# Kernel optimization log

Hardware: AMD Instinct MI355X
Metric: run time of the kernel (lower is better)

Reference implementation:

```python
import jax, jax.numpy as jnp
import numpy as np

# Module config (matches init_kwargs)
IC, OC = 8, 16
KH, KW = 3, 3
H, W = 32, 32
PAD, STRIDE = 1, 1
PH, PW = H + 2 * PAD, W + 2 * PAD          # padded input dims: 34x34
OH = (PH - KH) // STRIDE + 1                # 32
OW = (PW - KW) // STRIDE + 1                # 32
B = 64                                       # batch of flattened ciphertext images


def _build_toeplitz(kernel: np.ndarray) -> np.ndarray:
    """approximate_toeplitz_multiple_channels: dense [OC*OH*OW, IC*PH*PW] matrix
    such that T @ vec(padded_x) == vec(conv2d(x, kernel))."""
    T = np.zeros((OC * OH * OW, IC * PH * PW), dtype=np.float32)
    oh, ow = np.meshgrid(np.arange(OH), np.arange(OW), indexing="ij")
    oh, ow = oh.ravel(), ow.ravel()
    for oc in range(OC):
        rows = (oc * OH + oh) * OW + ow
        for ic in range(IC):
            for kh in range(KH):
                for kw in range(KW):
                    cols = (ic * PH + oh * STRIDE + kh) * PW + (ow * STRIDE + kw)
                    T[rows, cols] = kernel[oc, ic, kh, kw]
    return T


def _build_pad_mat() -> np.ndarray:
    """create_padding_transformation_matrix: [IC*PH*PW, IC*H*W] 0/1 matrix that
    zero-pads the flattened image (homomorphic padding as a matmul)."""
    P = np.zeros((IC * PH * PW, IC * H * W), dtype=np.float32)
    ic, h, w = np.meshgrid(np.arange(IC), np.arange(H), np.arange(W), indexing="ij")
    rows = (ic * PH + h + PAD) * PW + (w + PAD)
    cols = (ic * H + h) * W + w
    P[rows.ravel(), cols.ravel()] = 1.0
    return P


def setup_inputs() -> dict:
    rng = np.random.default_rng(0)
    kernel = rng.standard_normal((OC, IC, KH, KW)).astype(np.float32)
    weight = jnp.asarray(_build_toeplitz(kernel))                 # [OC*OH*OW, IC*PH*PW]
    bias = jnp.asarray(
        np.repeat(rng.standard_normal(OC).astype(np.float32), OH * OW)
    )                                                             # [OC*OH*OW]
    pad_mat = jnp.asarray(_build_pad_mat())                       # [IC*PH*PW, IC*H*W]
    key = jax.random.key(0)
    enc_x = jax.random.normal(key, (B, IC * H * W), dtype=jnp.float32)
    return {"enc_x": enc_x, "weight": weight, "bias": bias, "pad_mat": pad_mat}


def reference(enc_x, weight, bias, pad_mat):
    # Homomorphic conv as plaintext-equivalent math:
    # 1) pad via transformation matrix, 2) Toeplitz matmul, 3) add repeated bias.
    x_padded = enc_x @ pad_mat.T            # [B, IC*PH*PW]
    return x_padded @ weight.T + bias       # [B, OC*OH*OW]
```

## Files before the change

kernel.cpp:

```cpp
#include <hip/hip_runtime.h>

#define IC    8
#define OC    16
#define H     32
#define W     32
#define PH    34
#define PW    34
#define OH    32
#define OW    32
#define BATCH 64
#define WCOLS (IC * PH * PW)
#define XSTR  35
#define PLANE (PH * XSTR)

__global__ __launch_bounds__(256) void conv_toeplitz_kernel(
    const float* __restrict__ x,
    const float* __restrict__ weight,
    const float* __restrict__ bias,
    float* __restrict__ out)
{
    __shared__ float wk[IC * 9];
    __shared__ float xs[IC * PLANE];

    const int tid = threadIdx.x;
    const int blk = blockIdx.x;
    const int b   = blk >> 4;
    const int oc  = blk & 15;

    if (tid < IC * 9) {
        const int ic = tid / 9;
        const int k  = tid - ic * 9;
        const int kh = k / 3;
        const int kw = k - kh * 3;
        wk[tid] = weight[(size_t)(oc * OH * OW) * WCOLS + (ic * PH + kh) * PW + kw];
    }

    for (int i = tid; i < IC * PLANE; i += 256) xs[i] = 0.0f;
    __syncthreads();

    const float4* xg = (const float4*)(x + (size_t)b * (IC * H * W));
    #pragma unroll
    for (int i = 0; i < 8; ++i) {
        const int k   = tid + i * 256;
        const float4 v = xg[k];
        const int ic  = k >> 8;
        const int rem = k & 255;
        const int h   = rem >> 3;
        const int w4  = (rem & 7) << 2;
        float* dst = &xs[ic * PLANE + (h + 1) * XSTR + (w4 + 1)];
        dst[0] = v.x; dst[1] = v.y; dst[2] = v.z; dst[3] = v.w;
    }
    __syncthreads();

    float wreg[IC][3][3];
    #pragma unroll
    for (int ic = 0; ic < IC; ++ic)
        #pragma unroll
        for (int kh = 0; kh < 3; ++kh)
            #pragma unroll
            for (int kw = 0; kw < 3; ++kw)
                wreg[ic][kh][kw] = wk[ic * 9 + kh * 3 + kw];

    const int oh   = tid >> 3;
    const int ow0  = (tid & 7) << 2;
    const int oidx = oh * OW + ow0;

    const float4 bv = *(const float4*)(bias + oc * OH * OW + oidx);
    float acc0 = bv.x, acc1 = bv.y, acc2 = bv.z, acc3 = bv.w;

    #pragma unroll
    for (int ic = 0; ic < IC; ++ic) {
        #pragma unroll
        for (int kh = 0; kh < 3; ++kh) {
            const float* row = &xs[ic * PLANE + (oh + kh) * XSTR + ow0];
            const float v0 = row[0], v1 = row[1], v2 = row[2];
            const float v3 = row[3], v4 = row[4], v5 = row[5];
            const float w0 = wreg[ic][kh][0];
            const float w1 = wreg[ic][kh][1];
            const float w2 = wreg[ic][kh][2];
            acc0 += v0 * w0 + v1 * w1 + v2 * w2;
            acc1 += v1 * w0 + v2 * w1 + v3 * w2;
            acc2 += v2 * w0 + v3 * w1 + v4 * w2;
            acc3 += v3 * w0 + v4 * w1 + v5 * w2;
        }
    }

    float* op = out + (size_t)(b * OC + oc) * (OH * OW) + oidx;
    *(float4*)op = make_float4(acc0, acc1, acc2, acc3);
}

extern "C" void kernel_launch(void* const* d_in, const int* in_sizes, int n_in,
                              void* d_out, int out_size, void* d_ws, size_t ws_size,
                              hipStream_t stream) {
    const float* x      = (const float*)d_in[0];
    const float* weight = (const float*)d_in[1];
    const float* bias   = (const float*)d_in[2];
    float* out = (float*)d_out;

    conv_toeplitz_kernel<<<dim3(BATCH * OC), dim3(256), 0, stream>>>(x, weight, bias, out);
}
```

Baseline: 12.78 us.

## Compute two output channels per block and zero only the halo

Each block now computes two output channels for one image, so the staged input plane in shared memory is loaded once and reused for both, and the grid shrinks from 1024 to 512 blocks. Only the padding border is zeroed instead of the whole shared buffer, which also removes one barrier. Launch bounds now request two blocks per CU. The trade-off is more registers per thread (two weight sets and twice the accumulators) and fewer blocks to spread across the CUs.

```diff
diff --git a/kernel.cpp b/kernel.cpp
--- a/kernel.cpp
+++ b/kernel.cpp
@@ -12,31 +12,43 @@
 #define WCOLS (IC * PH * PW)
 #define XSTR  35
 #define PLANE (PH * XSTR)
+#define HALO  134
 
-__global__ __launch_bounds__(256) void conv_toeplitz_kernel(
+__global__ __launch_bounds__(256, 2) void conv_toeplitz_kernel(
     const float* __restrict__ x,
     const float* __restrict__ weight,
     const float* __restrict__ bias,
     float* __restrict__ out)
 {
-    __shared__ float wk[IC * 9];
+    __shared__ float wk[2][IC * 9];
     __shared__ float xs[IC * PLANE];
 
     const int tid = threadIdx.x;
     const int blk = blockIdx.x;
-    const int b   = blk >> 4;
-    const int oc  = blk & 15;
+    const int b   = blk >> 3;
+    const int oc0 = (blk & 7) << 1;
 
-    if (tid < IC * 9) {
-        const int ic = tid / 9;
-        const int k  = tid - ic * 9;
-        const int kh = k / 3;
-        const int kw = k - kh * 3;
-        wk[tid] = weight[(size_t)(oc * OH * OW) * WCOLS + (ic * PH + kh) * PW + kw];
+    if (tid < 144) {
+        const int os = tid / 72;
+        const int k  = tid - os * 72;
+        const int ic = k / 9;
+        const int r  = k - ic * 9;
+        const int kh = r / 3;
+        const int kw = r - kh * 3;
+        wk[os][k] = weight[(size_t)((oc0 + os) * OH * OW) * WCOLS
+                           + (ic * PH + kh) * PW + kw];
     }
 
-    for (int i = tid; i < IC * PLANE; i += 256) xs[i] = 0.0f;
-    __syncthreads();
+    for (int i = tid; i < IC * HALO; i += 256) {
+        const int plane = i / HALO;
+        const int r     = i - plane * HALO;
+        int row, col;
+        if (r < 35)       { row = 0;          col = r;        }
+        else if (r < 70)  { row = 33;         col = r - 35;   }
+        else if (r < 102) { row = r - 70 + 1; col = 0;        }
+        else              { row = r - 102 + 1; col = 33;      }
+        xs[plane * PLANE + row * XSTR + col] = 0.0f;
+    }
 
     const float4* xg = (const float4*)(x + (size_t)b * (IC * H * W));
     #pragma unroll
@@ -52,21 +64,21 @@
     }
     __syncthreads();
 
-    float wreg[IC][3][3];
+    float wreg[2][IC * 9];
     #pragma unroll
-    for (int ic = 0; ic < IC; ++ic)
+    for (int o = 0; o < 2; ++o)
         #pragma unroll
-        for (int kh = 0; kh < 3; ++kh)
-            #pragma unroll
-            for (int kw = 0; kw < 3; ++kw)
-                wreg[ic][kh][kw] = wk[ic * 9 + kh * 3 + kw];
+        for (int k = 0; k < IC * 9; ++k)
+            wreg[o][k] = wk[o][k];
 
     const int oh   = tid >> 3;
     const int ow0  = (tid & 7) << 2;
     const int oidx = oh * OW + ow0;
 
-    const float4 bv = *(const float4*)(bias + oc * OH * OW + oidx);
-    float acc0 = bv.x, acc1 = bv.y, acc2 = bv.z, acc3 = bv.w;
+    const float4 b0 = *(const float4*)(bias + oc0 * OH * OW + oidx);
+    const float4 b1 = *(const float4*)(bias + (oc0 + 1) * OH * OW + oidx);
+    float a00 = b0.x, a01 = b0.y, a02 = b0.z, a03 = b0.w;
+    float a10 = b1.x, a11 = b1.y, a12 = b1.z, a13 = b1.w;
 
     #pragma unroll
     for (int ic = 0; ic < IC; ++ic) {
@@ -75,18 +87,27 @@
             const float* row = &xs[ic * PLANE + (oh + kh) * XSTR + ow0];
             const float v0 = row[0], v1 = row[1], v2 = row[2];
             const float v3 = row[3], v4 = row[4], v5 = row[5];
-            const float w0 = wreg[ic][kh][0];
-            const float w1 = wreg[ic][kh][1];
-            const float w2 = wreg[ic][kh][2];
-            acc0 += v0 * w0 + v1 * w1 + v2 * w2;
-            acc1 += v1 * w0 + v2 * w1 + v3 * w2;
-            acc2 += v2 * w0 + v3 * w1 + v4 * w2;
-            acc3 += v3 * w0 + v4 * w1 + v5 * w2;
+            const float w00 = wreg[0][ic * 9 + kh * 3];
+            const float w01 = wreg[0][ic * 9 + kh * 3 + 1];
+            const float w02 = wreg[0][ic * 9 + kh * 3 + 2];
+            const float w10 = wreg[1][ic * 9 + kh * 3];
+            const float w11 = wreg[1][ic * 9 + kh * 3 + 1];
+            const float w12 = wreg[1][ic * 9 + kh * 3 + 2];
+            a00 += v0 * w00 + v1 * w01 + v2 * w02;
+            a01 += v1 * w00 + v2 * w01 + v3 * w02;
+            a02 += v2 * w00 + v3 * w01 + v4 * w02;
+            a03 += v3 * w00 + v4 * w01 + v5 * w02;
+            a10 += v0 * w10 + v1 * w11 + v2 * w12;
+            a11 += v1 * w10 + v2 * w11 + v3 * w12;
+            a12 += v2 * w10 + v3 * w11 + v4 * w12;
+            a13 += v3 * w10 + v4 * w11 + v5 * w12;
         }
     }
 
-    float* op = out + (size_t)(b * OC + oc) * (OH * OW) + oidx;
-    *(float4*)op = make_float4(acc0, acc1, acc2, acc3);
+    float* o0 = out + (size_t)(b * OC + oc0) * (OH * OW) + oidx;
+    *(float4*)o0 = make_float4(a00, a01, a02, a03);
+    float* o1 = o0 + OH * OW;
+    *(float4*)o1 = make_float4(a10, a11, a12, a13);
 }
 
 extern "C" void kernel_launch(void* const* d_in, const int* in_sizes, int n_in,
@@ -97,5 +118,5 @@
     const float* bias   = (const float*)d_in[2];
     float* out = (float*)d_out;
 
-    conv_toeplitz_kernel<<<dim3(BATCH * OC), dim3(256), 0, stream>>>(x, weight, bias, out);
+    conv_toeplitz_kernel<<<dim3(BATCH * (OC / 2)), dim3(256), 0, stream>>>(x, weight, bias, out);
 }
```

Result: faster. 10.94 us (-14.4%).

## Compute four output channels per block over half-image row tiles

Applied to the files above, without the earlier changes.

Each block now covers four output channels and half of the output rows (18 padded input rows), with 128 threads each producing a 4x4 register tile. Every input value loaded into shared memory is reused across four output channels, which cuts redundant input loads and shared-memory staging by roughly a factor of four. Only the halo borders are zeroed instead of the whole tile. The grid shrinks from 1024 to 512 blocks and each thread holds more accumulator and weight registers, which may reduce occupancy and latency hiding.

```diff
diff --git a/kernel.cpp b/kernel.cpp
--- a/kernel.cpp
+++ b/kernel.cpp
@@ -6,87 +6,107 @@
 #define W     32
 #define PH    34
 #define PW    34
-#define OH    32
-#define OW    32
 #define BATCH 64
 #define WCOLS (IC * PH * PW)
 #define XSTR  35
-#define PLANE (PH * XSTR)
+#define TROWS 18
+#define PLANE (TROWS * XSTR)
 
-__global__ __launch_bounds__(256) void conv_toeplitz_kernel(
+__global__ __launch_bounds__(128, 2) void conv_quad_kernel(
     const float* __restrict__ x,
     const float* __restrict__ weight,
     const float* __restrict__ bias,
     float* __restrict__ out)
 {
-    __shared__ float wk[IC * 9];
     __shared__ float xs[IC * PLANE];
+    __shared__ float wk[IC * 36];
 
-    const int tid = threadIdx.x;
+    const int t   = threadIdx.x;
     const int blk = blockIdx.x;
-    const int b   = blk >> 4;
-    const int oc  = blk & 15;
+    const int b   = blk >> 3;
+    const int q   = (blk >> 1) & 3;
+    const int hf  = blk & 1;
+    const int oc0 = q << 2;
+    const int dr0 = hf ? 15 : 0;
+    const int lr0 = hf ? 0 : 1;
+    const int lrh = hf ? 17 : 0;
+    const int oh0 = hf << 4;
 
-    if (tid < IC * 9) {
-        const int ic = tid / 9;
-        const int k  = tid - ic * 9;
+    for (int v = t; v < IC * 36; v += 128) {
+        const int ic = v / 36;
+        const int r  = v - ic * 36;
+        const int oc = r / 9;
+        const int k  = r - oc * 9;
         const int kh = k / 3;
         const int kw = k - kh * 3;
-        wk[tid] = weight[(size_t)(oc * OH * OW) * WCOLS + (ic * PH + kh) * PW + kw];
+        wk[v] = weight[(size_t)((oc0 + oc) << 10) * WCOLS + (ic * PH + kh) * PW + kw];
     }
 
-    for (int i = tid; i < IC * PLANE; i += 256) xs[i] = 0.0f;
-    __syncthreads();
+    #pragma unroll
+    for (int ic = 0; ic < IC; ++ic) {
+        if (t < 71) {
+            int row, col;
+            if (t < 36) { row = t >> 1; col = (t & 1) ? 33 : 0; }
+            else        { row = lrh;    col = t - 36; }
+            xs[ic * PLANE + row * XSTR + col] = 0.0f;
+        }
+    }
 
-    const float4* xg = (const float4*)(x + (size_t)b * (IC * H * W));
+    const float4* xg = (const float4*)(x + ((size_t)b << 13));
     #pragma unroll
-    for (int i = 0; i < 8; ++i) {
-        const int k   = tid + i * 256;
-        const float4 v = xg[k];
-        const int ic  = k >> 8;
-        const int rem = k & 255;
-        const int h   = rem >> 3;
-        const int w4  = (rem & 7) << 2;
-        float* dst = &xs[ic * PLANE + (h + 1) * XSTR + (w4 + 1)];
-        dst[0] = v.x; dst[1] = v.y; dst[2] = v.z; dst[3] = v.w;
+    for (int ic = 0; ic < IC; ++ic) {
+        for (int j = t; j < 136; j += 128) {
+            const int h  = j >> 3;
+            const int w4 = (j & 7) << 2;
+            const float4 v = xg[(ic << 8) + ((dr0 + h) << 3) + (j & 7)];
+            float* dst = &xs[ic * PLANE + (lr0 + h) * XSTR + w4 + 1];
+            dst[0] = v.x; dst[1] = v.y; dst[2] = v.z; dst[3] = v.w;
+        }
     }
     __syncthreads();
 
-    float wreg[IC][3][3];
+    const int r   = t >> 3;
+    const int ow0 = (t & 7) << 2;
+
+    float acc[4][4];
     #pragma unroll
-    for (int ic = 0; ic < IC; ++ic)
+    for (int oc = 0; oc < 4; ++oc)
         #pragma unroll
-        for (int kh = 0; kh < 3; ++kh)
-            #pragma unroll
-            for (int kw = 0; kw < 3; ++kw)
-                wreg[ic][kh][kw] = wk[ic * 9 + kh * 3 + kw];
-
-    const int oh   = tid >> 3;
-    const int ow0  = (tid & 7) << 2;
-    const int oidx = oh * OW + ow0;
-
-    const float4 bv = *(const float4*)(bias + oc * OH * OW + oidx);
-    float acc0 = bv.x, acc1 = bv.y, acc2 = bv.z, acc3 = bv.w;
+        for (int j = 0; j < 4; ++j) acc[oc][j] = 0.0f;
 
     #pragma unroll
     for (int ic = 0; ic < IC; ++ic) {
+        float w[36];
+        #pragma unroll
+        for (int i = 0; i < 9; ++i)
+            *(float4*)&w[i * 4] = *(const float4*)&wk[ic * 36 + i * 4];
+
         #pragma unroll
         for (int kh = 0; kh < 3; ++kh) {
-            const float* row = &xs[ic * PLANE + (oh + kh) * XSTR + ow0];
-            const float v0 = row[0], v1 = row[1], v2 = row[2];
-            const float v3 = row[3], v4 = row[4], v5 = row[5];
-            const float w0 = wreg[ic][kh][0];
-            const float w1 = wreg[ic][kh][1];
-            const float w2 = wreg[ic][kh][2];
-            acc0 += v0 * w0 + v1 * w1 + v2 * w2;
-            acc1 += v1 * w0 + v2 * w1 + v3 * w2;
-            acc2 += v2 * w0 + v3 * w1 + v4 * w2;
-            acc3 += v3 * w0 + v4 * w1 + v5 * w2;
+            const float* rp = &xs[ic * PLANE + (r + kh) * XSTR + ow0];
+            const float v0 = rp[0], v1 = rp[1], v2 = rp[2];
+            const float v3 = rp[3], v4 = rp[4], v5 = rp[5];
+            #pragma unroll
+            for (int oc = 0; oc < 4; ++oc) {
+                const float w0 = w[oc * 9 + kh * 3];
+                const float w1 = w[oc * 9 + kh * 3 + 1];
+                const float w2 = w[oc * 9 + kh * 3 + 2];
+                acc[oc][0] += v0 * w0 + v1 * w1 + v2 * w2;
+                acc[oc][1] += v1 * w0 + v2 * w1 + v3 * w2;
+                acc[oc][2] += v2 * w0 + v3 * w1 + v4 * w2;
+                acc[oc][3] += v3 * w0 + v4 * w1 + v5 * w2;
+            }
         }
     }
 
-    float* op = out + (size_t)(b * OC + oc) * (OH * OW) + oidx;
-    *(float4*)op = make_float4(acc0, acc1, acc2, acc3);
+    const int oidx = ((oh0 + r) << 5) + ow0;
+    #pragma unroll
+    for (int oc = 0; oc < 4; ++oc) {
+        const float4 bv = *(const float4*)(bias + ((oc0 + oc) << 10) + oidx);
+        float4 o = make_float4(acc[oc][0] + bv.x, acc[oc][1] + bv.y,
+                               acc[oc][2] + bv.z, acc[oc][3] + bv.w);
+        *(float4*)(out + (size_t)(((b << 4) + oc0 + oc) << 10) + oidx) = o;
+    }
 }
 
 extern "C" void kernel_launch(void* const* d_in, const int* in_sizes, int n_in,
@@ -97,5 +117,5 @@
     const float* bias   = (const float*)d_in[2];
     float* out = (float*)d_out;
 
-    conv_toeplitz_kernel<<<dim3(BATCH * OC), dim3(256), 0, stream>>>(x, weight, bias, out);
+    conv_quad_kernel<<<dim3(BATCH * 8), dim3(128), 0, stream>>>(x, weight, bias, out);
 }
```

Result: slower. 14.03 us (+9.8%).

## Drop shared-memory staging; compute two output channels per thread from global loads

Applied to the files above, without the earlier changes.

Replaces the LDS-staged padded input tile with direct global (cached) loads of each thread's 3x6 input window, handling padding with predicated clamps. Each block now covers half the spatial rows for two output channels using 128 threads, so every input window is reused across two channels. The weights are read as wave-uniform scalar loads through readfirstlane. This removes the LDS zero-fill, the stores into LDS and both barriers, in exchange for redundant global/L1 reads of overlapping rows and smaller blocks.

```diff
diff --git a/kernel.cpp b/kernel.cpp
--- a/kernel.cpp
+++ b/kernel.cpp
@@ -4,89 +4,88 @@
 #define OC    16
 #define H     32
 #define W     32
-#define PH    34
-#define PW    34
-#define OH    32
-#define OW    32
 #define BATCH 64
-#define WCOLS (IC * PH * PW)
-#define XSTR  35
-#define PLANE (PH * XSTR)
+#define WCOLS 9248
 
-__global__ __launch_bounds__(256) void conv_toeplitz_kernel(
+__global__ __launch_bounds__(128) void conv_direct_kernel(
     const float* __restrict__ x,
     const float* __restrict__ weight,
     const float* __restrict__ bias,
     float* __restrict__ out)
 {
-    __shared__ float wk[IC * 9];
-    __shared__ float xs[IC * PLANE];
-
     const int tid = threadIdx.x;
     const int blk = blockIdx.x;
     const int b   = blk >> 4;
-    const int oc  = blk & 15;
+    const int sub = blk & 15;
+    const int oc0 = (sub >> 1) << 1;
+    const int hf  = sub & 1;
+    const int oh  = (hf << 4) + (tid >> 3);
+    const int ow0 = (tid & 7) << 2;
 
-    if (tid < IC * 9) {
-        const int ic = tid / 9;
-        const int k  = tid - ic * 9;
-        const int kh = k / 3;
-        const int kw = k - kh * 3;
-        wk[tid] = weight[(size_t)(oc * OH * OW) * WCOLS + (ic * PH + kh) * PW + kw];
-    }
+    const float* xb = x + ((size_t)b << 13);
 
-    for (int i = tid; i < IC * PLANE; i += 256) xs[i] = 0.0f;
-    __syncthreads();
-
-    const float4* xg = (const float4*)(x + (size_t)b * (IC * H * W));
-    #pragma unroll
-    for (int i = 0; i < 8; ++i) {
-        const int k   = tid + i * 256;
-        const float4 v = xg[k];
-        const int ic  = k >> 8;
-        const int rem = k & 255;
-        const int h   = rem >> 3;
-        const int w4  = (rem & 7) << 2;
-        float* dst = &xs[ic * PLANE + (h + 1) * XSTR + (w4 + 1)];
-        dst[0] = v.x; dst[1] = v.y; dst[2] = v.z; dst[3] = v.w;
-    }
-    __syncthreads();
-
-    float wreg[IC][3][3];
-    #pragma unroll
-    for (int ic = 0; ic < IC; ++ic)
-        #pragma unroll
-        for (int kh = 0; kh < 3; ++kh)
-            #pragma unroll
-            for (int kw = 0; kw < 3; ++kw)
-                wreg[ic][kh][kw] = wk[ic * 9 + kh * 3 + kw];
-
-    const int oh   = tid >> 3;
-    const int ow0  = (tid & 7) << 2;
-    const int oidx = oh * OW + ow0;
-
-    const float4 bv = *(const float4*)(bias + oc * OH * OW + oidx);
-    float acc0 = bv.x, acc1 = bv.y, acc2 = bv.z, acc3 = bv.w;
+    float a0[4] = {0.f, 0.f, 0.f, 0.f};
+    float a1[4] = {0.f, 0.f, 0.f, 0.f};
 
     #pragma unroll
     for (int ic = 0; ic < IC; ++ic) {
+        float wv[2][9];
+        #pragma unroll
+        for (int os = 0; os < 2; ++os) {
+            const int wbase = __builtin_amdgcn_readfirstlane(
+                (oc0 + os) * (WCOLS << 10) + ic * 1156);
+            #pragma unroll
+            for (int kh = 0; kh < 3; ++kh)
+                #pragma unroll
+                for (int kw = 0; kw < 3; ++kw)
+                    wv[os][kh * 3 + kw] = weight[(size_t)wbase + kh * 34 + kw];
+        }
+
+        float w6[3][6];
+        #pragma unroll
+        for (int rr = 0; rr < 3; ++rr) {
+            const int  row = oh + rr - 1;
+            const bool ok  = (row >= 0) && (row < H);
+            const int  rc  = (row < 0) ? 0 : ((row > 31) ? 31 : row);
+            const float* bp = xb + (ic << 10) + (rc << 5) + ow0;
+            const float4 c  = *(const float4*)bp;
+            const float  lf = *(bp + (ow0 > 0 ? -1 : 0));
+            const float  rt = *(bp + (ow0 < 28 ? 4 : 0));
+            w6[rr][0] = (ok && ow0 > 0)  ? lf  : 0.f;
+            w6[rr][1] = ok ? c.x : 0.f;
+            w6[rr][2] = ok ? c.y : 0.f;
+            w6[rr][3] = ok ? c.z : 0.f;
+            w6[rr][4] = ok ? c.w : 0.f;
+            w6[rr][5] = (ok && ow0 < 28) ? rt  : 0.f;
+        }
+
         #pragma unroll
         for (int kh = 0; kh < 3; ++kh) {
-            const float* row = &xs[ic * PLANE + (oh + kh) * XSTR + ow0];
-            const float v0 = row[0], v1 = row[1], v2 = row[2];
-            const float v3 = row[3], v4 = row[4], v5 = row[5];
-            const float w0 = wreg[ic][kh][0];
-            const float w1 = wreg[ic][kh][1];
-            const float w2 = wreg[ic][kh][2];
-            acc0 += v0 * w0 + v1 * w1 + v2 * w2;
-            acc1 += v1 * w0 + v2 * w1 + v3 * w2;
-            acc2 += v2 * w0 + v3 * w1 + v4 * w2;
-            acc3 += v3 * w0 + v4 * w1 + v5 * w2;
+            const float v0 = w6[kh][0], v1 = w6[kh][1], v2 = w6[kh][2];
+            const float v3 = w6[kh][3], v4 = w6[kh][4], v5 = w6[kh][5];
+            {
+                const float w0 = wv[0][kh * 3], w1 = wv[0][kh * 3 + 1], w2 = wv[0][kh * 3 + 2];
+                a0[0] += v0 * w0 + v1 * w1 + v2 * w2;
+                a0[1] += v1 * w0 + v2 * w1 + v3 * w2;
+                a0[2] += v2 * w0 + v3 * w1 + v4 * w2;
+                a0[3] += v3 * w0 + v4 * w1 + v5 * w2;
+            }
+            {
+                const float w0 = wv[1][kh * 3], w1 = wv[1][kh * 3 + 1], w2 = wv[1][kh * 3 + 2];
+                a1[0] += v0 * w0 + v1 * w1 + v2 * w2;
+                a1[1] += v1 * w0 + v2 * w1 + v3 * w2;
+                a1[2] += v2 * w0 + v3 * w1 + v4 * w2;
+                a1[3] += v3 * w0 + v4 * w1 + v5 * w2;
+            }
         }
     }
 
-    float* op = out + (size_t)(b * OC + oc) * (OH * OW) + oidx;
-    *(float4*)op = make_float4(acc0, acc1, acc2, acc3);
+    const int oidx = (oh << 5) + ow0;
+    const float4 b0 = *(const float4*)(bias + (oc0 << 10) + oidx);
+    const float4 b1 = *(const float4*)(bias + ((oc0 + 1) << 10) + oidx);
+    float* op = out + (size_t)(((b << 4) + oc0) << 10) + oidx;
+    *(float4*)op          = make_float4(a0[0] + b0.x, a0[1] + b0.y, a0[2] + b0.z, a0[3] + b0.w);
+    *(float4*)(op + 1024) = make_float4(a1[0] + b1.x, a1[1] + b1.y, a1[2] + b1.z, a1[3] + b1.w);
 }
 
 extern "C" void kernel_launch(void* const* d_in, const int* in_sizes, int n_in,
@@ -97,5 +96,5 @@
     const float* bias   = (const float*)d_in[2];
     float* out = (float*)d_out;
 
-    conv_toeplitz_kernel<<<dim3(BATCH * OC), dim3(256), 0, stream>>>(x, weight, bias, out);
+    conv_direct_kernel<<<dim3(BATCH * 16), dim3(128), 0, stream>>>(x, weight, bias, out);
 }
```

Result: slower. 13.64 us (+6.7%).
